# Kernel tuning notes

Measured on AMD Instinct MI355X. Metric: run time of the kernel, lower is better.

The kernel has to match this reference:

```python
import jax, jax.numpy as jnp
import numpy as np

N_NODES = 50000
N_EDGES = 800000
IN_DIM, HID_DIM, OUT_DIM = 256, 128, 64


def gcn_conv(x, edge_index, W, b):
    """PyG GCNConv: out = D^{-1/2} (A + I) D^{-1/2} (x @ W) + b."""
    n = x.shape[0]
    loops = jnp.arange(n, dtype=edge_index.dtype)
    src = jnp.concatenate([edge_index[0], loops])  # message source j
    dst = jnp.concatenate([edge_index[1], loops])  # aggregation target i
    ones = jnp.ones(src.shape[0], dtype=x.dtype)
    deg = jax.ops.segment_sum(ones, dst, num_segments=n)  # >= 1 (self-loops)
    dinv = jax.lax.rsqrt(deg)
    norm = dinv[src] * dinv[dst]                    # [E+N]
    h = x @ W                                       # [N, out] GEMM first (PyG order)
    msg = h[src] * norm[:, None]                    # gather + scale
    out = jax.ops.segment_sum(msg, dst, num_segments=n)  # scatter-add
    return out + b


def setup_inputs() -> dict:
    key = jax.random.key(0)
    k1, k2, k3, k4, k5 = jax.random.split(key, 5)
    x = jax.random.normal(k1, (N_NODES, IN_DIM), dtype=jnp.float32)
    edge_index = jax.random.randint(k2, (2, N_EDGES), 0, N_NODES, dtype=jnp.int64)
    # Glorot-ish init for weights, zero bias (PyG defaults)
    W1 = jax.random.normal(k3, (IN_DIM, HID_DIM), dtype=jnp.float32) / np.sqrt(IN_DIM)
    b1 = jnp.zeros((HID_DIM,), dtype=jnp.float32)
    W2 = jax.random.normal(k4, (HID_DIM, OUT_DIM), dtype=jnp.float32) / np.sqrt(HID_DIM)
    b2 = jnp.zeros((OUT_DIM,), dtype=jnp.float32)
    return {"x": x, "edge_index": edge_index, "W1": W1, "b1": b1, "W2": W2, "b2": b2}


def reference(x, edge_index, W1, b1, W2, b2):
    h = jax.nn.relu(gcn_conv(x, edge_index, W1, b1))
    return gcn_conv(h, edge_index, W2, b2)
```

## Files before the change

kernel.cpp:

```cpp
#include <hip/hip_runtime.h>

#define N_NODES 50000
#define N_EDGES 800000
#define IN_DIM 256
#define HID_DIM 128
#define OUT_DIM 64
#define CAP 64

#define K_BINS 256
#define NPB 196
#define BINCAP 4096
#define CHUNK 2048
#define N_BINWG 391
#define N_WBLK 160
#define N_G1BLK 782

typedef __bf16 bf16x8 __attribute__((ext_vector_type(8)));
typedef float f32x4 __attribute__((ext_vector_type(4)));
typedef unsigned short u16x8 __attribute__((ext_vector_type(8)));
typedef unsigned short ushort_t;
typedef unsigned int uint_t;

__device__ __forceinline__ ushort_t f2bf(float f) {
    uint_t u = __float_as_uint(f);
    return (ushort_t)((u + 0x7fffu + ((u >> 16) & 1u)) >> 16);
}
__device__ __forceinline__ float bf_lo(uint_t u) { return __uint_as_float(u << 16); }
__device__ __forceinline__ float bf_hi(uint_t u) { return __uint_as_float(u & 0xffff0000u); }

__global__ __launch_bounds__(256) void k_binit(const float* __restrict__ W1,
                                               ushort_t* __restrict__ w1t,
                                               const float* __restrict__ W2,
                                               ushort_t* __restrict__ w2t,
                                               const int* __restrict__ srcs,
                                               const int* __restrict__ dsts,
                                               int* __restrict__ bin_cur,
                                               uint_t* __restrict__ binbuf) {
    const int bid = blockIdx.x;
    const int t = threadIdx.x;
    if (bid < N_WBLK) {
        if (bid < 128) {
            int id = bid * 256 + t;
            int k = id >> 7, c = id & 127;
            w1t[c * IN_DIM + k] = f2bf(W1[id]);
        } else {
            int id = (bid - 128) * 256 + t;
            int k = id >> 6, c = id & 63;
            w2t[c * HID_DIM + k] = f2bf(W2[id]);
        }
        return;
    }
    __shared__ int lcnt[K_BINS];
    __shared__ int lbase[K_BINS];
    lcnt[t] = 0;
    __syncthreads();
    const int start = (bid - N_WBLK) * CHUNK;
    int b_[8]; int p_[8]; uint_t rec_[8];
#pragma unroll
    for (int k = 0; k < 8; ++k) {
        int e = start + t + k * 256;
        bool ok = (e < N_EDGES);
        int d = ok ? dsts[e] : 0;
        int s = ok ? srcs[e] : 0;
        int b = d / NPB;
        b_[k] = ok ? b : -1;
        p_[k] = ok ? atomicAdd(&lcnt[b], 1) : 0;
        rec_[k] = (uint_t)s | ((uint_t)(d - b * NPB) << 16);
    }
    __syncthreads();
    lbase[t] = atomicAdd(&bin_cur[t], lcnt[t]);
    __syncthreads();
#pragma unroll
    for (int k = 0; k < 8; ++k) {
        if (b_[k] >= 0) {
            int pos = lbase[b_[k]] + p_[k];
            if (pos < BINCAP) binbuf[(size_t)b_[k] * BINCAP + pos] = rec_[k];
        }
    }
}

__global__ __launch_bounds__(256) void k_fillg1(const int* __restrict__ bin_cur,
                                                const uint_t* __restrict__ binbuf,
                                                ushort_t* __restrict__ es,
                                                float* __restrict__ dinv,
                                                int* __restrict__ ndeg,
                                                const float* __restrict__ x,
                                                const ushort_t* __restrict__ w1t,
                                                ushort_t* __restrict__ hb) {
    const int bid = blockIdx.x;
    const int t = threadIdx.x;
    if (bid < K_BINS) {
        __shared__ int cnt[NPB];
        __shared__ __align__(16) ushort_t pay[NPB][CAP];
        const int b = bid;
        if (t < NPB) cnt[t] = 0;
        __syncthreads();
        const int n = min(bin_cur[b], BINCAP);
        const uint_t* rec = binbuf + (size_t)b * BINCAP;
        const int base = t * 16;
        uint4 q0, q1, q2, q3;
        if (base < n) {
            const uint4* rp = (const uint4*)(rec + base);
            q0 = rp[0]; q1 = rp[1]; q2 = rp[2]; q3 = rp[3];
        }
#define SCAT(val, idx)                                                    \
        do {                                                              \
            if ((idx) < n) {                                              \
                uint_t rr = (val);                                        \
                int dl = rr >> 16;                                        \
                int p = atomicAdd(&cnt[dl], 1);                           \
                if (p < CAP) pay[dl][p] = (ushort_t)(rr & 0xffffu);       \
            }                                                             \
        } while (0)
        SCAT(q0.x, base + 0);  SCAT(q0.y, base + 1);
        SCAT(q0.z, base + 2);  SCAT(q0.w, base + 3);
        SCAT(q1.x, base + 4);  SCAT(q1.y, base + 5);
        SCAT(q1.z, base + 6);  SCAT(q1.w, base + 7);
        SCAT(q2.x, base + 8);  SCAT(q2.y, base + 9);
        SCAT(q2.z, base + 10); SCAT(q2.w, base + 11);
        SCAT(q3.x, base + 12); SCAT(q3.y, base + 13);
        SCAT(q3.z, base + 14); SCAT(q3.w, base + 15);
#undef SCAT
        __syncthreads();
        uint4* gdst = (uint4*)(es + (size_t)b * NPB * CAP);
        const uint4* lsrc = (const uint4*)&pay[0][0];
        for (int i = t; i < NPB * CAP / 8; i += 256) gdst[i] = lsrc[i];
        if (t < NPB) {
            int node = b * NPB + t;
            if (node < N_NODES) {
                int deg = cnt[t];
                dinv[node] = rsqrtf((float)(deg + 1));
                ndeg[node] = min(deg, CAP);
            }
        }
        return;
    }
    const int wave = t >> 6;
    const int lane = t & 63;
    const int l15 = lane & 15, quad = lane >> 4;
    const int tbase = (bid - K_BINS) * 64 + wave * 16;
    const int row = min(tbase + l15, N_NODES - 1);
    f32x4 acc[8];
#pragma unroll
    for (int n = 0; n < 8; ++n) acc[n] = (f32x4){0.f, 0.f, 0.f, 0.f};
    const float* xrow = x + (size_t)row * IN_DIM + quad * 8;
    const ushort_t* wbase = w1t + quad * 8;
#pragma unroll
    for (int tk = 0; tk < 8; ++tk) {
        const float4* xp = (const float4*)(xrow + tk * 32);
        float4 f0 = xp[0], f1 = xp[1];
        u16x8 au;
        au[0] = f2bf(f0.x); au[1] = f2bf(f0.y); au[2] = f2bf(f0.z); au[3] = f2bf(f0.w);
        au[4] = f2bf(f1.x); au[5] = f2bf(f1.y); au[6] = f2bf(f1.z); au[7] = f2bf(f1.w);
        bf16x8 a = __builtin_bit_cast(bf16x8, au);
#pragma unroll
        for (int n = 0; n < 8; ++n) {
            bf16x8 b = *(const bf16x8*)(wbase + (n * 16 + l15) * IN_DIM + tk * 32);
            acc[n] = __builtin_amdgcn_mfma_f32_16x16x32_bf16(a, b, acc[n], 0, 0, 0);
        }
    }
    const int row0 = tbase + quad * 4;
    ushort_t* hrow = hb + (size_t)row0 * HID_DIM + l15;
#pragma unroll
    for (int n = 0; n < 8; ++n)
#pragma unroll
        for (int r = 0; r < 4; ++r)
            if (row0 + r < N_NODES)
                hrow[(size_t)r * HID_DIM + n * 16] = f2bf(acc[n][r]);
}

__global__ __launch_bounds__(256) void k_agg1(const ushort_t* __restrict__ hb,
                                              const int* __restrict__ ndeg,
                                              const float* __restrict__ dinv,
                                              const ushort_t* __restrict__ es,
                                              const float* __restrict__ b,
                                              ushort_t* __restrict__ hrelu) {
    const int i = blockIdx.x * 4 + (threadIdx.x >> 6);
    const int lane = threadIdx.x & 63;
    const int half = lane >> 5;
    const int c = lane & 31;
    const float dv = dinv[i];
    const int n = ndeg[i];
    int   sj = 0;
    float nmj = 0.f;
    if (lane < n) {
        sj = (int)__builtin_nontemporal_load(&es[i * CAP + lane]);
        nmj = dinv[sj] * dv;
    }
    float a0 = 0.f, a1 = 0.f, a2 = 0.f, a3 = 0.f;
    int j = 0;
    for (; j + 16 <= n; j += 16) {
        int   s0 = __shfl(sj, j + half),      s1 = __shfl(sj, j + 2 + half);
        int   s2 = __shfl(sj, j + 4 + half),  s3 = __shfl(sj, j + 6 + half);
        int   s4 = __shfl(sj, j + 8 + half),  s5 = __shfl(sj, j + 10 + half);
        int   s6 = __shfl(sj, j + 12 + half), s7 = __shfl(sj, j + 14 + half);
        float m0 = __shfl(nmj, j + half),      m1 = __shfl(nmj, j + 2 + half);
        float m2 = __shfl(nmj, j + 4 + half),  m3 = __shfl(nmj, j + 6 + half);
        float m4 = __shfl(nmj, j + 8 + half),  m5 = __shfl(nmj, j + 10 + half);
        float m6 = __shfl(nmj, j + 12 + half), m7 = __shfl(nmj, j + 14 + half);
        uint2 v0 = *(const uint2*)(hb + (size_t)s0 * HID_DIM + 4 * c);
        uint2 v1 = *(const uint2*)(hb + (size_t)s1 * HID_DIM + 4 * c);
        uint2 v2 = *(const uint2*)(hb + (size_t)s2 * HID_DIM + 4 * c);
        uint2 v3 = *(const uint2*)(hb + (size_t)s3 * HID_DIM + 4 * c);
        uint2 v4 = *(const uint2*)(hb + (size_t)s4 * HID_DIM + 4 * c);
        uint2 v5 = *(const uint2*)(hb + (size_t)s5 * HID_DIM + 4 * c);
        uint2 v6 = *(const uint2*)(hb + (size_t)s6 * HID_DIM + 4 * c);
        uint2 v7 = *(const uint2*)(hb + (size_t)s7 * HID_DIM + 4 * c);
        a0 += bf_lo(v0.x) * m0 + bf_lo(v1.x) * m1 + bf_lo(v2.x) * m2 + bf_lo(v3.x) * m3
            + bf_lo(v4.x) * m4 + bf_lo(v5.x) * m5 + bf_lo(v6.x) * m6 + bf_lo(v7.x) * m7;
        a1 += bf_hi(v0.x) * m0 + bf_hi(v1.x) * m1 + bf_hi(v2.x) * m2 + bf_hi(v3.x) * m3
            + bf_hi(v4.x) * m4 + bf_hi(v5.x) * m5 + bf_hi(v6.x) * m6 + bf_hi(v7.x) * m7;
        a2 += bf_lo(v0.y) * m0 + bf_lo(v1.y) * m1 + bf_lo(v2.y) * m2 + bf_lo(v3.y) * m3
            + bf_lo(v4.y) * m4 + bf_lo(v5.y) * m5 + bf_lo(v6.y) * m6 + bf_lo(v7.y) * m7;
        a3 += bf_hi(v0.y) * m0 + bf_hi(v1.y) * m1 + bf_hi(v2.y) * m2 + bf_hi(v3.y) * m3
            + bf_hi(v4.y) * m4 + bf_hi(v5.y) * m5 + bf_hi(v6.y) * m6 + bf_hi(v7.y) * m7;
    }
    for (; j < n; j += 2) {
        int   s = __shfl(sj, j + half);
        float m = __shfl(nmj, j + half);
        uint2 v = *(const uint2*)(hb + (size_t)s * HID_DIM + 4 * c);
        a0 += bf_lo(v.x) * m; a1 += bf_hi(v.x) * m;
        a2 += bf_lo(v.y) * m; a3 += bf_hi(v.y) * m;
    }
    a0 += __shfl_xor(a0, 32); a1 += __shfl_xor(a1, 32);
    a2 += __shfl_xor(a2, 32); a3 += __shfl_xor(a3, 32);
    if (lane < 32) {
        uint2 u = *(const uint2*)(hb + (size_t)i * HID_DIM + 4 * c);
        const float dvv = dv * dv;
        float r0 = a0 + bf_lo(u.x) * dvv + b[4 * c];
        float r1 = a1 + bf_hi(u.x) * dvv + b[4 * c + 1];
        float r2 = a2 + bf_lo(u.y) * dvv + b[4 * c + 2];
        float r3 = a3 + bf_hi(u.y) * dvv + b[4 * c + 3];
        r0 = fmaxf(r0, 0.f); r1 = fmaxf(r1, 0.f);
        r2 = fmaxf(r2, 0.f); r3 = fmaxf(r3, 0.f);
        uint2 o;
        o.x = ((uint_t)f2bf(r1) << 16) | f2bf(r0);
        o.y = ((uint_t)f2bf(r3) << 16) | f2bf(r2);
        *(uint2*)(hrelu + (size_t)i * HID_DIM + 4 * c) = o;
    }
}

__global__ __launch_bounds__(256) void k_gemm2(const ushort_t* __restrict__ hrelu,
                                               const ushort_t* __restrict__ w2t,
                                               ushort_t* __restrict__ h2) {
    const int t = threadIdx.x;
    const int wave = t >> 6;
    const int lane = t & 63;
    const int l15 = lane & 15, quad = lane >> 4;
    const int tbase = blockIdx.x * 64 + wave * 16;
    const int row = min(tbase + l15, N_NODES - 1);
    f32x4 acc[4];
#pragma unroll
    for (int n = 0; n < 4; ++n) acc[n] = (f32x4){0.f, 0.f, 0.f, 0.f};
    const ushort_t* arow = hrelu + (size_t)row * HID_DIM + quad * 8;
    const ushort_t* wbase = w2t + quad * 8;
#pragma unroll
    for (int tk = 0; tk < 4; ++tk) {
        bf16x8 a = *(const bf16x8*)(arow + tk * 32);
#pragma unroll
        for (int n = 0; n < 4; ++n) {
            bf16x8 b = *(const bf16x8*)(wbase + (n * 16 + l15) * HID_DIM + tk * 32);
            acc[n] = __builtin_amdgcn_mfma_f32_16x16x32_bf16(a, b, acc[n], 0, 0, 0);
        }
    }
    const int row0 = tbase + quad * 4;
    ushort_t* orow = h2 + (size_t)row0 * OUT_DIM + l15;
#pragma unroll
    for (int n = 0; n < 4; ++n)
#pragma unroll
        for (int r = 0; r < 4; ++r)
            if (row0 + r < N_NODES)
                orow[(size_t)r * OUT_DIM + n * 16] = f2bf(acc[n][r]);
}

__global__ __launch_bounds__(256) void k_agg2(const ushort_t* __restrict__ h2,
                                              const int* __restrict__ ndeg,
                                              const float* __restrict__ dinv,
                                              const ushort_t* __restrict__ es,
                                              const float* __restrict__ b,
                                              float* __restrict__ out) {
    const int i = blockIdx.x * 4 + (threadIdx.x >> 6);
    const int lane = threadIdx.x & 63;
    const int half = lane >> 5;
    const int c = lane & 31;
    const float dv = dinv[i];
    const int n = ndeg[i];
    int   sj = 0;
    float nmj = 0.f;
    if (lane < n) {
        sj = (int)__builtin_nontemporal_load(&es[i * CAP + lane]);
        nmj = dinv[sj] * dv;
    }
    float a0 = 0.f, a1 = 0.f;
    int j = 0;
    for (; j + 16 <= n; j += 16) {
        int   s0 = __shfl(sj, j + half),      s1 = __shfl(sj, j + 2 + half);
        int   s2 = __shfl(sj, j + 4 + half),  s3 = __shfl(sj, j + 6 + half);
        int   s4 = __shfl(sj, j + 8 + half),  s5 = __shfl(sj, j + 10 + half);
        int   s6 = __shfl(sj, j + 12 + half), s7 = __shfl(sj, j + 14 + half);
        float m0 = __shfl(nmj, j + half),      m1 = __shfl(nmj, j + 2 + half);
        float m2 = __shfl(nmj, j + 4 + half),  m3 = __shfl(nmj, j + 6 + half);
        float m4 = __shfl(nmj, j + 8 + half),  m5 = __shfl(nmj, j + 10 + half);
        float m6 = __shfl(nmj, j + 12 + half), m7 = __shfl(nmj, j + 14 + half);
        uint_t v0 = *(const uint_t*)(h2 + (size_t)s0 * OUT_DIM + 2 * c);
        uint_t v1 = *(const uint_t*)(h2 + (size_t)s1 * OUT_DIM + 2 * c);
        uint_t v2 = *(const uint_t*)(h2 + (size_t)s2 * OUT_DIM + 2 * c);
        uint_t v3 = *(const uint_t*)(h2 + (size_t)s3 * OUT_DIM + 2 * c);
        uint_t v4 = *(const uint_t*)(h2 + (size_t)s4 * OUT_DIM + 2 * c);
        uint_t v5 = *(const uint_t*)(h2 + (size_t)s5 * OUT_DIM + 2 * c);
        uint_t v6 = *(const uint_t*)(h2 + (size_t)s6 * OUT_DIM + 2 * c);
        uint_t v7 = *(const uint_t*)(h2 + (size_t)s7 * OUT_DIM + 2 * c);
        a0 += bf_lo(v0) * m0 + bf_lo(v1) * m1 + bf_lo(v2) * m2 + bf_lo(v3) * m3
            + bf_lo(v4) * m4 + bf_lo(v5) * m5 + bf_lo(v6) * m6 + bf_lo(v7) * m7;
        a1 += bf_hi(v0) * m0 + bf_hi(v1) * m1 + bf_hi(v2) * m2 + bf_hi(v3) * m3
            + bf_hi(v4) * m4 + bf_hi(v5) * m5 + bf_hi(v6) * m6 + bf_hi(v7) * m7;
    }
    for (; j < n; j += 2) {
        int   s = __shfl(sj, j + half);
        float m = __shfl(nmj, j + half);
        uint_t v = *(const uint_t*)(h2 + (size_t)s * OUT_DIM + 2 * c);
        a0 += bf_lo(v) * m;
        a1 += bf_hi(v) * m;
    }
    a0 += __shfl_xor(a0, 32);
    a1 += __shfl_xor(a1, 32);
    if (lane < 32) {
        uint_t u = *(const uint_t*)(h2 + (size_t)i * OUT_DIM + 2 * c);
        float2 r;
        r.x = a0 + bf_lo(u) * dv * dv + b[2 * c];
        r.y = a1 + bf_hi(u) * dv * dv + b[2 * c + 1];
        *(float2*)(out + (size_t)i * OUT_DIM + 2 * c) = r;
    }
}

extern "C" void kernel_launch(void* const* d_in, const int* in_sizes, int n_in,
                              void* d_out, int out_size, void* d_ws, size_t ws_size,
                              hipStream_t stream) {
    const float* x   = (const float*)d_in[0];
    const int*   ei  = (const int*)d_in[1];
    const float* W1  = (const float*)d_in[2];
    const float* b1  = (const float*)d_in[3];
    const float* W2  = (const float*)d_in[4];
    const float* b2  = (const float*)d_in[5];
    float* out = (float*)d_out;

    const int* srcs = ei;
    const int* dsts = ei + N_EDGES;

    char* ws = (char*)d_ws;
    size_t o = 0;
    auto alloc = [&](size_t bytes) { void* p = ws + o; o = (o + bytes + 511) & ~size_t(511); return p; };
    int*      bin_cur = (int*)   alloc(K_BINS * 4);
    float*    dinv  = (float*)   alloc(N_NODES * 4);
    int*      ndeg  = (int*)     alloc(N_NODES * 4);
    ushort_t* es    = (ushort_t*)alloc((size_t)K_BINS * NPB * CAP * 2);
    uint_t*   binbuf= (uint_t*)  alloc((size_t)K_BINS * BINCAP * 4);
    ushort_t* w1t   = (ushort_t*)alloc((size_t)IN_DIM * HID_DIM * 2);
    ushort_t* w2t   = (ushort_t*)alloc((size_t)HID_DIM * OUT_DIM * 2);
    ushort_t* hb    = (ushort_t*)alloc((size_t)N_NODES * HID_DIM * 2);
    ushort_t* hrelu = (ushort_t*)alloc((size_t)N_NODES * HID_DIM * 2);
    ushort_t* h2    = (ushort_t*)alloc((size_t)N_NODES * OUT_DIM * 2);

    hipMemsetAsync(bin_cur, 0, K_BINS * 4, stream);
    k_binit <<<N_WBLK + N_BINWG, 256, 0, stream>>>(W1, w1t, W2, w2t, srcs, dsts, bin_cur, binbuf);
    k_fillg1<<<K_BINS + N_G1BLK, 256, 0, stream>>>(bin_cur, binbuf, es, dinv, ndeg, x, w1t, hb);
    k_agg1  <<<N_NODES / 4, 256, 0, stream>>>(hb, ndeg, dinv, es, b1, hrelu);
    k_gemm2 <<<N_G1BLK, 256, 0, stream>>>(hrelu, w2t, h2);
    k_agg2  <<<N_NODES / 4, 256, 0, stream>>>(h2, ndeg, dinv, es, b2, out);
}
```

Measured before the change: 222.0 us.

## Split fused fill/GEMM1 kernel and hoist all A-operand loads ahead of MFMAs

Splits the combined bin-fill plus first-GEMM kernel into two separate launches, so the GEMM blocks no longer reserve the fill path's large shared-memory footprint and can reach higher occupancy. In both GEMM kernels, all activation loads for a row are issued up front before the MFMA chain, giving more memory-level parallelism. The cost is an extra kernel launch and the loss of overlap between the fill and GEMM work, plus higher register pressure from holding all the loaded x values at once.

New measurement: 227.0 us. +2.3%, slower.

```diff
diff --git a/kernel.cpp b/kernel.cpp
--- a/kernel.cpp
+++ b/kernel.cpp
@@ -79,86 +79,101 @@
     }
 }
 
-__global__ __launch_bounds__(256) void k_fillg1(const int* __restrict__ bin_cur,
-                                                const uint_t* __restrict__ binbuf,
-                                                ushort_t* __restrict__ es,
-                                                float* __restrict__ dinv,
-                                                int* __restrict__ ndeg,
-                                                const float* __restrict__ x,
-                                                const ushort_t* __restrict__ w1t,
-                                                ushort_t* __restrict__ hb) {
-    const int bid = blockIdx.x;
+__global__ __launch_bounds__(256) void k_fill(const int* __restrict__ bin_cur,
+                                              const uint_t* __restrict__ binbuf,
+                                              ushort_t* __restrict__ es,
+                                              float* __restrict__ dinv,
+                                              int* __restrict__ ndeg) {
+    __shared__ int cnt[NPB];
+    __shared__ __align__(16) ushort_t pay[NPB][CAP];
+    const int b = blockIdx.x, t = threadIdx.x;
+    if (t < NPB) cnt[t] = 0;
+    __syncthreads();
+    const int n = min(bin_cur[b], BINCAP);
+    const uint_t* rec = binbuf + (size_t)b * BINCAP;
+    const int base = t * 16;
+    uint4 q0, q1, q2, q3;
+    if (base < n) {
+        const uint4* rp = (const uint4*)(rec + base);
+        q0 = rp[0]; q1 = rp[1]; q2 = rp[2]; q3 = rp[3];
+    }
+#define SCAT(val, idx)                                                    \
+    do {                                                                  \
+        if ((idx) < n) {                                                  \
+            uint_t rr = (val);                                            \
+            int dl = rr >> 16;                                            \
+            int p = atomicAdd(&cnt[dl], 1);                               \
+            if (p < CAP) pay[dl][p] = (ushort_t)(rr & 0xffffu);           \
+        }                                                                 \
+    } while (0)
+    SCAT(q0.x, base + 0);  SCAT(q0.y, base + 1);
+    SCAT(q0.z, base + 2);  SCAT(q0.w, base + 3);
+    SCAT(q1.x, base + 4);  SCAT(q1.y, base + 5);
+    SCAT(q1.z, base + 6);  SCAT(q1.w, base + 7);
+    SCAT(q2.x, base + 8);  SCAT(q2.y, base + 9);
+    SCAT(q2.z, base + 10); SCAT(q2.w, base + 11);
+    SCAT(q3.x, base + 12); SCAT(q3.y, base + 13);
+    SCAT(q3.z, base + 14); SCAT(q3.w, base + 15);
+#undef SCAT
+    __syncthreads();
+    uint4* gdst = (uint4*)(es + (size_t)b * NPB * CAP);
+    const uint4* lsrc = (const uint4*)&pay[0][0];
+    for (int i = t; i < NPB * CAP / 8; i += 256) gdst[i] = lsrc[i];
+    if (t < NPB) {
+        int node = b * NPB + t;
+        if (node < N_NODES) {
+            int deg = cnt[t];
+            dinv[node] = rsqrtf((float)(deg + 1));
+            ndeg[node] = min(deg, CAP);
+        }
+    }
+}
+
+__global__ __launch_bounds__(256) void k_gemm1(const float* __restrict__ x,
+                                               const ushort_t* __restrict__ w1t,
+                                               ushort_t* __restrict__ hb) {
     const int t = threadIdx.x;
-    if (bid < K_BINS) {
-        __shared__ int cnt[NPB];
-        __shared__ __align__(16) ushort_t pay[NPB][CAP];
-        const int b = bid;
-        if (t < NPB) cnt[t] = 0;
-        __syncthreads();
-        const int n = min(bin_cur[b], BINCAP);
-        const uint_t* rec = binbuf + (size_t)b * BINCAP;
-        const int base = t * 16;
-        uint4 q0, q1, q2, q3;
-        if (base < n) {
-            const uint4* rp = (const uint4*)(rec + base);
-            q0 = rp[0]; q1 = rp[1]; q2 = rp[2]; q3 = rp[3];
-        }
-#define SCAT(val, idx)                                                    \
-        do {                                                              \
-            if ((idx) < n) {                                              \
-                uint_t rr = (val);                                        \
-                int dl = rr >> 16;                                        \
-                int p = atomicAdd(&cnt[dl], 1);                           \
-                if (p < CAP) pay[dl][p] = (ushort_t)(rr & 0xffffu);       \
-            }                                                             \
-        } while (0)
-        SCAT(q0.x, base + 0);  SCAT(q0.y, base + 1);
-        SCAT(q0.z, base + 2);  SCAT(q0.w, base + 3);
-        SCAT(q1.x, base + 4);  SCAT(q1.y, base + 5);
-        SCAT(q1.z, base + 6);  SCAT(q1.w, base + 7);
-        SCAT(q2.x, base + 8);  SCAT(q2.y, base + 9);
-        SCAT(q2.z, base + 10); SCAT(q2.w, base + 11);
-        SCAT(q3.x, base + 12); SCAT(q3.y, base + 13);
-        SCAT(q3.z, base + 14); SCAT(q3.w, base + 15);
-#undef SCAT
-        __syncthreads();
-        uint4* gdst = (uint4*)(es + (size_t)b * NPB * CAP);
-        const uint4* lsrc = (const uint4*)&pay[0][0];
-        for (int i = t; i < NPB * CAP / 8; i += 256) gdst[i] = lsrc[i];
-        if (t < NPB) {
-            int node = b * NPB + t;
-            if (node < N_NODES) {
-                int deg = cnt[t];
-                dinv[node] = rsqrtf((float)(deg + 1));
-                ndeg[node] = min(deg, CAP);
-            }
-        }
-        return;
-    }
     const int wave = t >> 6;
     const int lane = t & 63;
     const int l15 = lane & 15, quad = lane >> 4;
-    const int tbase = (bid - K_BINS) * 64 + wave * 16;
+    const int tbase = blockIdx.x * 64 + wave * 16;
     const int row = min(tbase + l15, N_NODES - 1);
+    const float* xrow = x + (size_t)row * IN_DIM + quad * 8;
+    float4 xa0 = *(const float4*)(xrow +   0), xb0 = *(const float4*)(xrow +   4);
+    float4 xa1 = *(const float4*)(xrow +  32), xb1 = *(const float4*)(xrow +  36);
+    float4 xa2 = *(const float4*)(xrow +  64), xb2 = *(const float4*)(xrow +  68);
+    float4 xa3 = *(const float4*)(xrow +  96), xb3 = *(const float4*)(xrow + 100);
+    float4 xa4 = *(const float4*)(xrow + 128), xb4 = *(const float4*)(xrow + 132);
+    float4 xa5 = *(const float4*)(xrow + 160), xb5 = *(const float4*)(xrow + 164);
+    float4 xa6 = *(const float4*)(xrow + 192), xb6 = *(const float4*)(xrow + 196);
+    float4 xa7 = *(const float4*)(xrow + 224), xb7 = *(const float4*)(xrow + 228);
     f32x4 acc[8];
 #pragma unroll
     for (int n = 0; n < 8; ++n) acc[n] = (f32x4){0.f, 0.f, 0.f, 0.f};
-    const float* xrow = x + (size_t)row * IN_DIM + quad * 8;
     const ushort_t* wbase = w1t + quad * 8;
-#pragma unroll
-    for (int tk = 0; tk < 8; ++tk) {
-        const float4* xp = (const float4*)(xrow + tk * 32);
-        float4 f0 = xp[0], f1 = xp[1];
-        u16x8 au;
-        au[0] = f2bf(f0.x); au[1] = f2bf(f0.y); au[2] = f2bf(f0.z); au[3] = f2bf(f0.w);
-        au[4] = f2bf(f1.x); au[5] = f2bf(f1.y); au[6] = f2bf(f1.z); au[7] = f2bf(f1.w);
-        bf16x8 a = __builtin_bit_cast(bf16x8, au);
-#pragma unroll
-        for (int n = 0; n < 8; ++n) {
-            bf16x8 b = *(const bf16x8*)(wbase + (n * 16 + l15) * IN_DIM + tk * 32);
-            acc[n] = __builtin_amdgcn_mfma_f32_16x16x32_bf16(a, b, acc[n], 0, 0, 0);
-        }
-    }
+#define G1STEP(tk, xa, xb)                                                        \
+    {                                                                             \
+        u16x8 au;                                                                 \
+        au[0] = f2bf(xa.x); au[1] = f2bf(xa.y);                                   \
+        au[2] = f2bf(xa.z); au[3] = f2bf(xa.w);                                   \
+        au[4] = f2bf(xb.x); au[5] = f2bf(xb.y);                                   \
+        au[6] = f2bf(xb.z); au[7] = f2bf(xb.w);                                   \
+        bf16x8 a = __builtin_bit_cast(bf16x8, au);                                \
+        _Pragma("unroll")                                                         \
+        for (int n = 0; n < 8; ++n) {                                             \
+            bf16x8 bb = *(const bf16x8*)(wbase + (n * 16 + l15) * IN_DIM + tk * 32); \
+            acc[n] = __builtin_amdgcn_mfma_f32_16x16x32_bf16(a, bb, acc[n], 0, 0, 0); \
+        }                                                                         \
+    }
+    G1STEP(0, xa0, xb0)
+    G1STEP(1, xa1, xb1)
+    G1STEP(2, xa2, xb2)
+    G1STEP(3, xa3, xb3)
+    G1STEP(4, xa4, xb4)
+    G1STEP(5, xa5, xb5)
+    G1STEP(6, xa6, xb6)
+    G1STEP(7, xa7, xb7)
+#undef G1STEP
     const int row0 = tbase + quad * 4;
     ushort_t* hrow = hb + (size_t)row0 * HID_DIM + l15;
 #pragma unroll
@@ -254,15 +269,23 @@
     for (int n = 0; n < 4; ++n) acc[n] = (f32x4){0.f, 0.f, 0.f, 0.f};
     const ushort_t* arow = hrelu + (size_t)row * HID_DIM + quad * 8;
     const ushort_t* wbase = w2t + quad * 8;
-#pragma unroll
-    for (int tk = 0; tk < 4; ++tk) {
-        bf16x8 a = *(const bf16x8*)(arow + tk * 32);
-#pragma unroll
-        for (int n = 0; n < 4; ++n) {
-            bf16x8 b = *(const bf16x8*)(wbase + (n * 16 + l15) * HID_DIM + tk * 32);
-            acc[n] = __builtin_amdgcn_mfma_f32_16x16x32_bf16(a, b, acc[n], 0, 0, 0);
-        }
-    }
+    bf16x8 a0 = *(const bf16x8*)(arow +  0);
+    bf16x8 a1 = *(const bf16x8*)(arow + 32);
+    bf16x8 a2 = *(const bf16x8*)(arow + 64);
+    bf16x8 a3 = *(const bf16x8*)(arow + 96);
+#define G2STEP(tk, a)                                                             \
+    {                                                                             \
+        _Pragma("unroll")                                                         \
+        for (int n = 0; n < 4; ++n) {                                             \
+            bf16x8 bb = *(const bf16x8*)(wbase + (n * 16 + l15) * HID_DIM + tk * 32); \
+            acc[n] = __builtin_amdgcn_mfma_f32_16x16x32_bf16(a, bb, acc[n], 0, 0, 0); \
+        }                                                                         \
+    }
+    G2STEP(0, a0)
+    G2STEP(1, a1)
+    G2STEP(2, a2)
+    G2STEP(3, a3)
+#undef G2STEP
     const int row0 = tbase + quad * 4;
     ushort_t* orow = h2 + (size_t)row0 * OUT_DIM + l15;
 #pragma unroll
@@ -363,7 +386,8 @@
 
     hipMemsetAsync(bin_cur, 0, K_BINS * 4, stream);
     k_binit <<<N_WBLK + N_BINWG, 256, 0, stream>>>(W1, w1t, W2, w2t, srcs, dsts, bin_cur, binbuf);
-    k_fillg1<<<K_BINS + N_G1BLK, 256, 0, stream>>>(bin_cur, binbuf, es, dinv, ndeg, x, w1t, hb);
+    k_gemm1 <<<N_G1BLK, 256, 0, stream>>>(x, w1t, hb);
+    k_fill  <<<K_BINS, 256, 0, stream>>>(bin_cur, binbuf, es, dinv, ndeg);
     k_agg1  <<<N_NODES / 4, 256, 0, stream>>>(hb, ndeg, dinv, es, b1, hrelu);
     k_gemm2 <<<N_G1BLK, 256, 0, stream>>>(hrelu, w2t, h2);
     k_agg2  <<<N_NODES / 4, 256, 0, stream>>>(h2, ndeg, dinv, es, b2, out);
```
